# Optimization experiments

Measured on AMD Instinct MI355X. Metric: run time of the kernel, lower is better.

## Reference

```python
import jax, jax.numpy as jnp
import numpy as np

B = 16384
HIST_LEN, DYN_DIM, STAT_DIM, TIME_DIM = 24, 8, 3, 8
N_STATIONS, EMB_DIM = 120, 16
IN_DIM = HIST_LEN * DYN_DIM + STAT_DIM + TIME_DIM + EMB_DIM  # 219
HIDDEN, OUT = 64, 1
GRID, K = 5, 3
NUM_BASIS = GRID + K  # 8


def make_grid(in_dim):
    # uniform extended grid on [-1, 1], pykan-style: G + 2k + 1 knots per input
    h = 2.0 / GRID
    pts = jnp.arange(-K, GRID + K + 1, dtype=jnp.float32) * h - 1.0  # [G+2k+1]
    return jnp.broadcast_to(pts, (in_dim, pts.shape[0]))


def b_splines(x, grid_pts):
    # x: [B, I], grid_pts: [I, G+2k+1] -> bases [B, I, G+k] via Cox-de Boor
    g = grid_pts[None]              # [1, I, M]
    xe = x[..., None]               # [B, I, 1]
    b = ((xe >= g[..., :-1]) & (xe < g[..., 1:])).astype(x.dtype)
    for p in range(1, K + 1):
        b = ((xe - g[..., : -(p + 1)]) / (g[..., p:-1] - g[..., : -(p + 1)]) * b[..., :-1]
             + (g[..., p + 1:] - xe) / (g[..., p + 1:] - g[..., 1:-p]) * b[..., 1:])
    return b  # [B, I, G+k]


def kan_layer(x, w_base, coef, grid_pts):
    # base path (silu residual) + spline path
    y_base = jax.nn.silu(x) @ w_base                              # [B, O]
    y_spline = jnp.einsum('big,iog->bo', b_splines(x, grid_pts), coef)
    return y_base + y_spline


def setup_inputs() -> dict:
    key = jax.random.key(0)
    ks = jax.random.split(key, 9)
    hist = jax.random.normal(ks[0], (B, HIST_LEN, DYN_DIM), dtype=jnp.float32)
    static = jax.random.normal(ks[1], (B, STAT_DIM), dtype=jnp.float32)
    time_feats = jax.random.normal(ks[2], (B, TIME_DIM), dtype=jnp.float32)
    st_idx = jax.random.randint(ks[3], (B,), 0, N_STATIONS)
    emb_table = jax.random.normal(ks[4], (N_STATIONS, EMB_DIM), dtype=jnp.float32)
    s1 = 1.0 / np.sqrt(IN_DIM)
    s2 = 1.0 / np.sqrt(HIDDEN)
    w_base1 = jax.random.normal(ks[5], (IN_DIM, HIDDEN), dtype=jnp.float32) * s1
    coef1 = jax.random.normal(ks[6], (IN_DIM, HIDDEN, NUM_BASIS), dtype=jnp.float32) * (0.1 * s1)
    w_base2 = jax.random.normal(ks[7], (HIDDEN, OUT), dtype=jnp.float32) * s2
    coef2 = jax.random.normal(ks[8], (HIDDEN, OUT, NUM_BASIS), dtype=jnp.float32) * (0.1 * s2)
    return {"hist": hist, "static": static, "time_feats": time_feats, "st_idx": st_idx,
            "emb_table": emb_table, "w_base1": w_base1, "coef1": coef1,
            "w_base2": w_base2, "coef2": coef2}


def reference(hist, static, time_feats, st_idx, emb_table, w_base1, coef1, w_base2, coef2):
    grid1 = make_grid(IN_DIM)
    grid2 = make_grid(HIDDEN)
    hist_flat = hist.reshape(hist.shape[0], -1)          # [B, hist_len*dyn_dim]
    emb = emb_table[st_idx]                              # [B, emb_dim]
    x = jnp.concatenate([hist_flat, static, time_feats, emb], axis=1)  # [B, 219]
    h = kan_layer(x, w_base1, coef1, grid1)              # [B, 64]
    out = kan_layer(h, w_base2, coef2, grid2)            # [B, 1]
    return out.squeeze(-1)                               # [B]
```

## Files before the change

kernel.cpp:

```cpp
#include <hip/hip_runtime.h>


typedef _Float16 half8 __attribute__((ext_vector_type(8)));
typedef float floatx4 __attribute__((ext_vector_type(4)));

#define XR 233

__device__ __forceinline__ float silu_f(float x) {
    return x / (1.0f + __expf(-x));
}

__device__ __forceinline__ void bspline8_dense(float x, float f[8]) {
    float u  = (x + 2.2f) * 2.5f;
    float fj = floorf(u);
    float t  = u - fj;
    int   j  = (int)fj;
    bool valid = (u >= 0.0f) && (u < 11.0f);
    float t2 = t * t, t3 = t2 * t, omt = 1.0f - t;
    float b0 = omt * omt * omt * (1.0f / 6.0f);
    float b1 = (3.0f * t3 - 6.0f * t2 + 4.0f) * (1.0f / 6.0f);
    float b2 = (-3.0f * t3 + 3.0f * t2 + 3.0f * t + 1.0f) * (1.0f / 6.0f);
    float b3 = t3 * (1.0f / 6.0f);
    if (!valid) { b0 = b1 = b2 = b3 = 0.0f; }
    int base = j - 3;
#pragma unroll
    for (int g = 0; g < 8; ++g) {
        int m = g - base;
        float v = (m == 0) ? b0 : 0.0f;
        v = (m == 1) ? b1 : v;
        v = (m == 2) ? b2 : v;
        v = (m == 3) ? b3 : v;
        f[g] = v;
    }
}

__device__ __forceinline__ half8 bspline_frag(float x) {
    float u  = (x + 2.2f) * 2.5f;
    float fj = floorf(u);
    float t  = u - fj;
    int   j  = (int)fj;
    bool valid = (u >= 0.0f) && (u < 11.0f);
    float t2 = t * t, t3 = t2 * t, omt = 1.0f - t;
    float b0 = omt * omt * omt * (1.0f / 6.0f);
    float b1 = (3.0f * t3 - 6.0f * t2 + 4.0f) * (1.0f / 6.0f);
    float b2 = (-3.0f * t3 + 3.0f * t2 + 3.0f * t + 1.0f) * (1.0f / 6.0f);
    float b3 = t3 * (1.0f / 6.0f);
    union { _Float16 h[4]; unsigned long long q; } p;
    p.h[0] = (_Float16)b0; p.h[1] = (_Float16)b1;
    p.h[2] = (_Float16)b2; p.h[3] = (_Float16)b3;
    unsigned long long lo = valid ? p.q : 0ull;
    int jc = valid ? j : 3;
    int sh = (jc - 3) * 16;
    unsigned long long rlo, rhi;
    if (sh >= 0) {
        rlo = (sh < 64) ? (lo << sh) : 0ull;
        rhi = (sh == 0) ? 0ull
            : (sh < 64) ? (lo >> (64 - sh))
                        : (lo << (sh - 64));
    } else {
        rlo = lo >> (-sh);
        rhi = 0ull;
    }
    union { unsigned long long q[2]; half8 v; } r;
    r.q[0] = rlo; r.q[1] = rhi;
    return r.v;
}

__global__ __launch_bounds__(256) void build_w(
    const float* __restrict__ wb1, const float* __restrict__ cf1,
    _Float16* __restrict__ wcat)
{
    int flat = blockIdx.x * 256 + threadIdx.x;
    int lane = flat & 63;
    int nt   = (flat >> 6) & 3;
    int st   = flat >> 8;
    int kg   = lane >> 4;
    int n    = nt * 16 + (lane & 15);
    _Float16 v[8];
    if (st < 7) {
#pragma unroll
        for (int j = 0; j < 8; ++j) {
            int i = st * 32 + kg * 8 + j;
            v[j] = (_Float16)((i < 219) ? wb1[i * 64 + n] : 0.0f);
        }
    } else {
        int i = (st - 7) * 4 + kg;
#pragma unroll
        for (int j = 0; j < 8; ++j)
            v[j] = (_Float16)((i < 219) ? cf1[(i * 64 + n) * 8 + j] : 0.0f);
    }
    *(half8*)(wcat + (size_t)flat * 8) = *(half8*)v;
}

__global__ __launch_bounds__(256) void kan_mfma(
    const float* __restrict__ hist,
    const float* __restrict__ statf,
    const float* __restrict__ timef,
    const int*   __restrict__ st_idx,
    const float* __restrict__ emb,
    const _Float16* __restrict__ wcat,
    const float* __restrict__ wb2,
    const float* __restrict__ cf2,
    float* __restrict__ out)
{
    __shared__ union {
        float xb[32 * XR];
        struct { float h[2][32 * 65]; float part[8 * 32]; } ep;
    } sm;

    const int tid  = threadIdx.x;
    const int lane = tid & 63;
    const int w    = __builtin_amdgcn_readfirstlane(tid >> 6);
    const int mt   = w & 1;
    const int kh   = w >> 1;
    const int bx   = blockIdx.x;
    const int row  = lane & 15;
    const int kg   = lane >> 4;

    {
        const int s = tid >> 3, q4 = tid & 7;
        const int b = bx * 32 + s;
        const float4* h4 = (const float4*)hist;
#pragma unroll
        for (int f = 0; f < 6; ++f) {
            int i4 = q4 + 8 * f;
            float4 v = h4[b * 48 + i4];
            sm.xb[s * XR + i4 * 4 + 0] = v.x;
            sm.xb[s * XR + i4 * 4 + 1] = v.y;
            sm.xb[s * XR + i4 * 4 + 2] = v.z;
            sm.xb[s * XR + i4 * 4 + 3] = v.w;
        }
    }
#pragma unroll
    for (int f = 0; f < 4; ++f) {
        int flat = f * 256 + tid;
        int s  = flat >> 5;
        int ii = 192 + (flat & 31);
        int b  = bx * 32 + s;
        float v;
        if (ii < 195)      v = statf[b * 3 + (ii - 192)];
        else if (ii < 203) v = timef[b * 8 + (ii - 195)];
        else if (ii < 219) v = emb[st_idx[b] * 16 + (ii - 203)];
        else               v = 0.0f;
        sm.xb[s * XR + ii] = v;
    }
    __syncthreads();

    const float* xrow = &sm.xb[(mt * 16 + row) * XR];

    floatx4 acc[4];
#pragma unroll
    for (int nt = 0; nt < 4; ++nt) acc[nt] = (floatx4){0.f, 0.f, 0.f, 0.f};

    for (int st = kh; st < 7; st += 2) {
        const _Float16* wp = wcat + (size_t)(st * 4) * 512 + lane * 8;
        half8 bf0 = *(const half8*)(wp);
        half8 bf1 = *(const half8*)(wp + 512);
        half8 bf2 = *(const half8*)(wp + 1024);
        half8 bf3 = *(const half8*)(wp + 1536);
        const int i0 = st * 32 + kg * 8;
        half8 af;
#pragma unroll
        for (int jj = 0; jj < 8; ++jj)
            af[jj] = (_Float16)silu_f(xrow[i0 + jj]);
        acc[0] = __builtin_amdgcn_mfma_f32_16x16x32_f16(af, bf0, acc[0], 0, 0, 0);
        acc[1] = __builtin_amdgcn_mfma_f32_16x16x32_f16(af, bf1, acc[1], 0, 0, 0);
        acc[2] = __builtin_amdgcn_mfma_f32_16x16x32_f16(af, bf2, acc[2], 0, 0, 0);
        acc[3] = __builtin_amdgcn_mfma_f32_16x16x32_f16(af, bf3, acc[3], 0, 0, 0);
    }

    const int st0 = (kh == 1) ? 7 : 8;
#pragma unroll 2
    for (int st = st0; st < 63; st += 2) {
        const _Float16* wp = wcat + (size_t)(st * 4) * 512 + lane * 8;
        half8 bf0 = *(const half8*)(wp);
        half8 bf1 = *(const half8*)(wp + 512);
        half8 bf2 = *(const half8*)(wp + 1024);
        half8 bf3 = *(const half8*)(wp + 1536);
        float x = xrow[(st - 7) * 4 + kg];
        half8 af = bspline_frag(x);
        acc[0] = __builtin_amdgcn_mfma_f32_16x16x32_f16(af, bf0, acc[0], 0, 0, 0);
        acc[1] = __builtin_amdgcn_mfma_f32_16x16x32_f16(af, bf1, acc[1], 0, 0, 0);
        acc[2] = __builtin_amdgcn_mfma_f32_16x16x32_f16(af, bf2, acc[2], 0, 0, 0);
        acc[3] = __builtin_amdgcn_mfma_f32_16x16x32_f16(af, bf3, acc[3], 0, 0, 0);
    }

    __syncthreads();
#pragma unroll
    for (int nt = 0; nt < 4; ++nt) {
#pragma unroll
        for (int r = 0; r < 4; ++r) {
            const int rr = mt * 16 + kg * 4 + r;
            const int cc = nt * 16 + row;
            sm.ep.h[kh][rr * 65 + cc] = acc[nt][r];
        }
    }
    __syncthreads();

    {
        const int s  = tid & 31;
        const int og = tid >> 5;
        float psum = 0.0f;
#pragma unroll
        for (int oo = 0; oo < 8; ++oo) {
            const int o = og * 8 + oo;
            float h = sm.ep.h[0][s * 65 + o] + sm.ep.h[1][s * 65 + o];
            psum = fmaf(silu_f(h), wb2[o], psum);
            float f2[8];
            bspline8_dense(h, f2);
#pragma unroll
            for (int g = 0; g < 8; ++g)
                psum = fmaf(f2[g], cf2[o * 8 + g], psum);
        }
        sm.ep.part[og * 32 + s] = psum;
    }
    __syncthreads();
    if (tid < 32) {
        float r = 0.0f;
#pragma unroll
        for (int og = 0; og < 8; ++og) r += sm.ep.part[og * 32 + tid];
        out[bx * 32 + tid] = r;
    }
}

extern "C" void kernel_launch(void* const* d_in, const int* in_sizes, int n_in,
                              void* d_out, int out_size, void* d_ws, size_t ws_size,
                              hipStream_t stream) {
    const float* hist  = (const float*)d_in[0];
    const float* statf = (const float*)d_in[1];
    const float* timef = (const float*)d_in[2];
    const int*   stidx = (const int*)  d_in[3];
    const float* emb   = (const float*)d_in[4];
    const float* wb1   = (const float*)d_in[5];
    const float* cf1   = (const float*)d_in[6];
    const float* wb2   = (const float*)d_in[7];
    const float* cf2   = (const float*)d_in[8];
    float* out = (float*)d_out;

    _Float16* wcat = (_Float16*)d_ws;

    build_w<<<63, 256, 0, stream>>>(wb1, cf1, wcat);
    kan_mfma<<<512, 256, 0, stream>>>(hist, statf, timef, stidx, emb,
                                      wcat, wb2, cf2, out);
}
```

Baseline: 94.08 us.

## Split K across eight waves with register-resident weights and 64-row tiles

Each block now handles 64 samples with 512 threads. The K dimension (63 k-steps) is partitioned across 8 waves, and each wave preloads its 8 weight fragments into registers and reuses them across four 16-row M tiles. Per-wave partial accumulators are reduced with LDS atomicAdd into a zeroed shared buffer before the second-layer epilogue. This aims to cut repeated global weight fetches and raise MFMA reuse per load. In exchange it adds heavy register pressure (about 192 VGPRs for weights plus accumulators) and contended LDS atomics, and it launches fewer blocks.

```diff
diff --git a/kernel.cpp b/kernel.cpp
--- a/kernel.cpp
+++ b/kernel.cpp
@@ -4,7 +4,7 @@
 typedef _Float16 half8 __attribute__((ext_vector_type(8)));
 typedef float floatx4 __attribute__((ext_vector_type(4)));
 
-#define XR 233
+#define XR 236
 
 __device__ __forceinline__ float silu_f(float x) {
     return x / (1.0f + __expf(-x));
@@ -92,7 +92,7 @@
     *(half8*)(wcat + (size_t)flat * 8) = *(half8*)v;
 }
 
-__global__ __launch_bounds__(256) void kan_mfma(
+__global__ __launch_bounds__(512, 2) void kan_mfma(
     const float* __restrict__ hist,
     const float* __restrict__ statf,
     const float* __restrict__ timef,
@@ -104,27 +104,25 @@
     float* __restrict__ out)
 {
     __shared__ union {
-        float xb[32 * XR];
-        struct { float h[2][32 * 65]; float part[8 * 32]; } ep;
+        float xb[64 * XR];
+        struct { float h[64 * 65]; float part[8 * 64]; } ep;
     } sm;
 
     const int tid  = threadIdx.x;
     const int lane = tid & 63;
-    const int w    = __builtin_amdgcn_readfirstlane(tid >> 6);
-    const int mt   = w & 1;
-    const int kh   = w >> 1;
+    const int q    = __builtin_amdgcn_readfirstlane(tid >> 6);
     const int bx   = blockIdx.x;
-    const int row  = lane & 15;
+    const int c15  = lane & 15;
     const int kg   = lane >> 4;
 
     {
-        const int s = tid >> 3, q4 = tid & 7;
-        const int b = bx * 32 + s;
         const float4* h4 = (const float4*)hist;
 #pragma unroll
         for (int f = 0; f < 6; ++f) {
-            int i4 = q4 + 8 * f;
-            float4 v = h4[b * 48 + i4];
+            int flat = f * 512 + tid;
+            int s  = flat / 48;
+            int i4 = flat - s * 48;
+            float4 v = h4[(size_t)(bx * 64 + s) * 48 + i4];
             sm.xb[s * XR + i4 * 4 + 0] = v.x;
             sm.xb[s * XR + i4 * 4 + 1] = v.y;
             sm.xb[s * XR + i4 * 4 + 2] = v.z;
@@ -132,79 +130,78 @@
         }
     }
 #pragma unroll
-    for (int f = 0; f < 4; ++f) {
-        int flat = f * 256 + tid;
-        int s  = flat >> 5;
-        int ii = 192 + (flat & 31);
-        int b  = bx * 32 + s;
+    for (int f = 0; f < 6; ++f) {
+        int flat = f * 512 + tid;
+        int s  = flat / 48;
+        int ii = 192 + (flat - s * 48);
+        int b  = bx * 64 + s;
         float v;
         if (ii < 195)      v = statf[b * 3 + (ii - 192)];
         else if (ii < 203) v = timef[b * 8 + (ii - 195)];
         else if (ii < 219) v = emb[st_idx[b] * 16 + (ii - 203)];
         else               v = 0.0f;
-        sm.xb[s * XR + ii] = v;
-    }
-    __syncthreads();
-
-    const float* xrow = &sm.xb[(mt * 16 + row) * XR];
-
-    floatx4 acc[4];
-#pragma unroll
-    for (int nt = 0; nt < 4; ++nt) acc[nt] = (floatx4){0.f, 0.f, 0.f, 0.f};
-
-    for (int st = kh; st < 7; st += 2) {
-        const _Float16* wp = wcat + (size_t)(st * 4) * 512 + lane * 8;
-        half8 bf0 = *(const half8*)(wp);
-        half8 bf1 = *(const half8*)(wp + 512);
-        half8 bf2 = *(const half8*)(wp + 1024);
-        half8 bf3 = *(const half8*)(wp + 1536);
-        const int i0 = st * 32 + kg * 8;
-        half8 af;
-#pragma unroll
-        for (int jj = 0; jj < 8; ++jj)
-            af[jj] = (_Float16)silu_f(xrow[i0 + jj]);
-        acc[0] = __builtin_amdgcn_mfma_f32_16x16x32_f16(af, bf0, acc[0], 0, 0, 0);
-        acc[1] = __builtin_amdgcn_mfma_f32_16x16x32_f16(af, bf1, acc[1], 0, 0, 0);
-        acc[2] = __builtin_amdgcn_mfma_f32_16x16x32_f16(af, bf2, acc[2], 0, 0, 0);
-        acc[3] = __builtin_amdgcn_mfma_f32_16x16x32_f16(af, bf3, acc[3], 0, 0, 0);
-    }
-
-    const int st0 = (kh == 1) ? 7 : 8;
-#pragma unroll 2
-    for (int st = st0; st < 63; st += 2) {
-        const _Float16* wp = wcat + (size_t)(st * 4) * 512 + lane * 8;
-        half8 bf0 = *(const half8*)(wp);
-        half8 bf1 = *(const half8*)(wp + 512);
-        half8 bf2 = *(const half8*)(wp + 1024);
-        half8 bf3 = *(const half8*)(wp + 1536);
-        float x = xrow[(st - 7) * 4 + kg];
-        half8 af = bspline_frag(x);
-        acc[0] = __builtin_amdgcn_mfma_f32_16x16x32_f16(af, bf0, acc[0], 0, 0, 0);
-        acc[1] = __builtin_amdgcn_mfma_f32_16x16x32_f16(af, bf1, acc[1], 0, 0, 0);
-        acc[2] = __builtin_amdgcn_mfma_f32_16x16x32_f16(af, bf2, acc[2], 0, 0, 0);
-        acc[3] = __builtin_amdgcn_mfma_f32_16x16x32_f16(af, bf3, acc[3], 0, 0, 0);
-    }
-
-    __syncthreads();
-#pragma unroll
-    for (int nt = 0; nt < 4; ++nt) {
-#pragma unroll
-        for (int r = 0; r < 4; ++r) {
-            const int rr = mt * 16 + kg * 4 + r;
-            const int cc = nt * 16 + row;
-            sm.ep.h[kh][rr * 65 + cc] = acc[nt][r];
-        }
-    }
+        if (ii < XR) sm.xb[s * XR + ii] = v;
+    }
+    __syncthreads();
+
+    half8 breg[8][4];
+#pragma unroll
+    for (int u = 0; u < 8; ++u) {
+        const _Float16* wp = wcat + (size_t)(8 * u + q) * 2048 + lane * 8;
+#pragma unroll
+        for (int nt = 0; nt < 4; ++nt)
+            breg[u][nt] = *(const half8*)(wp + nt * 512);
+    }
+
+    floatx4 acc[4][4];
+#pragma unroll
+    for (int m = 0; m < 4; ++m)
+#pragma unroll
+        for (int nt = 0; nt < 4; ++nt) acc[m][nt] = (floatx4){0.f, 0.f, 0.f, 0.f};
+
+#pragma unroll
+    for (int u = 0; u < 8; ++u) {
+        const int st = 8 * u + q;
+#pragma unroll
+        for (int m = 0; m < 4; ++m) {
+            const float* xr = &sm.xb[(m * 16 + c15) * XR];
+            half8 af;
+            if (u == 0 && st < 7) {
+                const int i0 = st * 32 + kg * 8;
+#pragma unroll
+                for (int j = 0; j < 8; ++j)
+                    af[j] = (_Float16)silu_f(xr[i0 + j]);
+            } else {
+                af = bspline_frag(xr[(st - 7) * 4 + kg]);
+            }
+            acc[m][0] = __builtin_amdgcn_mfma_f32_16x16x32_f16(af, breg[u][0], acc[m][0], 0, 0, 0);
+            acc[m][1] = __builtin_amdgcn_mfma_f32_16x16x32_f16(af, breg[u][1], acc[m][1], 0, 0, 0);
+            acc[m][2] = __builtin_amdgcn_mfma_f32_16x16x32_f16(af, breg[u][2], acc[m][2], 0, 0, 0);
+            acc[m][3] = __builtin_amdgcn_mfma_f32_16x16x32_f16(af, breg[u][3], acc[m][3], 0, 0, 0);
+        }
+    }
+
+    __syncthreads();
+    for (int z = tid; z < 64 * 65; z += 512) sm.ep.h[z] = 0.0f;
+    __syncthreads();
+#pragma unroll
+    for (int m = 0; m < 4; ++m)
+#pragma unroll
+        for (int nt = 0; nt < 4; ++nt)
+#pragma unroll
+            for (int r = 0; r < 4; ++r)
+                atomicAdd(&sm.ep.h[(m * 16 + kg * 4 + r) * 65 + nt * 16 + c15],
+                          acc[m][nt][r]);
     __syncthreads();
 
     {
-        const int s  = tid & 31;
-        const int og = tid >> 5;
+        const int s  = tid & 63;
+        const int og = tid >> 6;
         float psum = 0.0f;
 #pragma unroll
         for (int oo = 0; oo < 8; ++oo) {
             const int o = og * 8 + oo;
-            float h = sm.ep.h[0][s * 65 + o] + sm.ep.h[1][s * 65 + o];
+            float h = sm.ep.h[s * 65 + o];
             psum = fmaf(silu_f(h), wb2[o], psum);
             float f2[8];
             bspline8_dense(h, f2);
@@ -212,14 +209,14 @@
             for (int g = 0; g < 8; ++g)
                 psum = fmaf(f2[g], cf2[o * 8 + g], psum);
         }
-        sm.ep.part[og * 32 + s] = psum;
-    }
-    __syncthreads();
-    if (tid < 32) {
+        sm.ep.part[og * 64 + s] = psum;
+    }
+    __syncthreads();
+    if (tid < 64) {
         float r = 0.0f;
 #pragma unroll
-        for (int og = 0; og < 8; ++og) r += sm.ep.part[og * 32 + tid];
-        out[bx * 32 + tid] = r;
+        for (int og = 0; og < 8; ++og) r += sm.ep.part[og * 64 + tid];
+        out[bx * 64 + tid] = r;
     }
 }
 
@@ -239,7 +236,7 @@
 
     _Float16* wcat = (_Float16*)d_ws;
 
-    build_w<<<63, 256, 0, stream>>>(wb1, cf1, wcat);
-    kan_mfma<<<512, 256, 0, stream>>>(hist, statf, timef, stidx, emb,
+    build_w<<<64, 256, 0, stream>>>(wb1, cf1, wcat);
+    kan_mfma<<<256, 512, 0, stream>>>(hist, statf, timef, stidx, emb,
                                       wcat, wb2, cf2, out);
 }
```

Result: slower. 137.2 us (+45.9%).
